# Kernel optimization log

Hardware: AMD Instinct MI355X
Metric: run time of the kernel (lower is better)

## Reference

```python
import jax, jax.numpy as jnp
import numpy as np

B, L, H, D = 4, 2048, 12, 64
CHUNK = 128  # chunk size for the causal linear-attention scan
EPS = 1e-6


def setup_inputs() -> dict:
    key = jax.random.key(0)
    kq, kk, kv = jax.random.split(key, 3)
    return {
        "q": jax.random.normal(kq, (B, L, H, D), jnp.float32),
        "k": jax.random.normal(kk, (B, L, H, D), jnp.float32),
        "v": jax.random.normal(kv, (B, L, H, D), jnp.float32),
    }


def _phi(x):
    # elu feature map: elu(x) + 1 (strictly positive)
    return jax.nn.elu(x) + 1.0


def _causal_linear(q, k, v):
    """Chunked causal linear attention numerator.
    out[l] = q[l] @ sum_{s<=l} k[s] (x) v[s].  q,k,v: [N,L,H,D]."""
    n, l, h, d = q.shape
    g = l // CHUNK
    qc = q.reshape(n, g, CHUNK, h, d)
    kc = k.reshape(n, g, CHUNK, h, d)
    vc = v.reshape(n, g, CHUNK, h, d)
    # per-chunk kv outer-product sums -> [N, G, H, D, M]
    kv = jnp.einsum('ngchd,ngchm->nghdm', kc, vc)
    # exclusive prefix sum over chunks (state entering each chunk)
    s_incl = jnp.cumsum(kv, axis=1)
    s_excl = jnp.concatenate([jnp.zeros_like(s_incl[:, :1]), s_incl[:, :-1]], axis=1)
    inter = jnp.einsum('ngchd,nghdm->ngchm', qc, s_excl)
    # intra-chunk causal part
    scores = jnp.einsum('ngchd,ngshd->ngchs', qc, kc)  # [N,G,C,H,C]
    mask = jnp.tril(jnp.ones((CHUNK, CHUNK), scores.dtype))  # s <= c
    scores = scores * mask.reshape(1, 1, CHUNK, 1, CHUNK)
    intra = jnp.einsum('ngchs,ngshm->ngchm', scores, vc)
    return (inter + intra).reshape(n, l, h, -1)


def reference(q, k, v):
    qf = _phi(q)
    kf = _phi(k)
    # normalizer z[n,l,h] = q[l] . cumsum_s<=l k[s]
    z = jnp.einsum('nlhd,nlhd->nlh', qf, jnp.cumsum(kf, axis=1)) + EPS
    num = _causal_linear(qf, kf, v)
    return num / z[..., None]
```

## Files before the change

### kernel.cpp

```cpp
#include <hip/hip_runtime.h>

#define NB 4
#define LL 2048
#define NH 12
#define DD 64
#define CB 128
#define NG (LL/CB)
#define NBH (NB*NH)
#define ST_BYTES (DD*DD*2)
#define KS_BASE_BYTES ((size_t)NBH*NG*ST_BYTES)

typedef short bf16x8 __attribute__((ext_vector_type(8)));
typedef float f32x4  __attribute__((ext_vector_type(4)));

#define SWZ8(row, x)  ((x) ^ (((row) & 7) << 4))
#define SWZ16(row, x) ((x) ^ (((row) & 15) << 4))

__device__ __forceinline__ float phi(float x) {
    return x > 0.0f ? x + 1.0f : __expf(x);
}
__device__ __forceinline__ unsigned f2bf1(float x) {
    union { float f; unsigned u; } v; v.f = x;
    return (v.u + 0x7FFFu + ((v.u >> 16) & 1u)) >> 16;
}
__device__ __forceinline__ unsigned packbf(float a, float b) {
    return f2bf1(a) | (f2bf1(b) << 16);
}
__device__ __forceinline__ float bf2f(unsigned short u) {
    union { unsigned u; float f; } v; v.u = ((unsigned)u) << 16; return v.f;
}
__device__ __forceinline__ void addbf8(float* run, uint4 a) {
    const unsigned u[4] = {a.x, a.y, a.z, a.w};
    #pragma unroll
    for (int i = 0; i < 4; ++i) {
        run[2*i+0] += bf2f((unsigned short)(u[i] & 0xffffu));
        run[2*i+1] += bf2f((unsigned short)(u[i] >> 16));
    }
}
__device__ __forceinline__ uint4 pack8(const float* run) {
    uint4 s;
    s.x = packbf(run[0], run[1]); s.y = packbf(run[2], run[3]);
    s.z = packbf(run[4], run[5]); s.w = packbf(run[6], run[7]);
    return s;
}

__global__ __launch_bounds__(256) void la_chunk_sums(
    const float* __restrict__ kin, const float* __restrict__ vin,
    char* __restrict__ wsb)
{
    __shared__ __align__(16) char sm[32768];
    const int bid = blockIdx.x;
    const int g = bid & (NG-1);
    const int h = (bid >> 4) % NH;
    const int n = bid / (NG*NH);
    const int t = threadIdx.x;
    const int l0 = g * CB;
    const int w = t >> 6, l = t & 63, gq = l >> 4, c16 = l & 15;

    #pragma unroll
    for (int p = 0; p < 8; ++p) {
        const int i = p*256 + t;
        const int r = i >> 4, c4 = i & 15;
        const size_t gidx = ((size_t)((n*LL + l0 + r)*NH + h))*DD + c4*4;
        float4 kk = *(const float4*)(kin + gidx);
        float4 vl = *(const float4*)(vin + gidx);
        const float kf[4] = {phi(kk.x), phi(kk.y), phi(kk.z), phi(kk.w)};
        const float vf[4] = {vl.x, vl.y, vl.z, vl.w};
        #pragma unroll
        for (int j = 0; j < 4; ++j) {
            const int d = c4*4 + j;
            *(unsigned short*)(sm +         d*256 + SWZ16(d, 2*r)) = (unsigned short)f2bf1(kf[j]);
            *(unsigned short*)(sm + 16384 + d*256 + SWZ16(d, 2*r)) = (unsigned short)f2bf1(vf[j]);
        }
    }
    __syncthreads();

    const int m = 16*w + c16;
    bf16x8 va[4];
    #pragma unroll
    for (int ks = 0; ks < 4; ++ks)
        va[ks] = *(const bf16x8*)(sm + 16384 + m*256 + SWZ16(m, 64*ks + 16*gq));
    const short one = (short)0x3F80;
    const bf16x8 ones = {one, one, one, one, one, one, one, one};

    f32x4 acc[4], ksa[4];
    #pragma unroll
    for (int td = 0; td < 4; ++td) {
        acc[td] = (f32x4){0.f,0.f,0.f,0.f};
        ksa[td] = (f32x4){0.f,0.f,0.f,0.f};
    }
    #pragma unroll
    for (int td = 0; td < 4; ++td) {
        const int d = 16*td + c16;
        #pragma unroll
        for (int ks = 0; ks < 4; ++ks) {
            const bf16x8 kb = *(const bf16x8*)(sm + d*256 + SWZ16(d, 64*ks + 16*gq));
            acc[td] = __builtin_amdgcn_mfma_f32_16x16x32_bf16(va[ks], kb, acc[td], 0, 0, 0);
            ksa[td] = __builtin_amdgcn_mfma_f32_16x16x32_bf16(ones,  kb, ksa[td], 0, 0, 0);
        }
    }

    char* stg = wsb + (size_t)bid * ST_BYTES;
    #pragma unroll
    for (int td = 0; td < 4; ++td)
        #pragma unroll
        for (int e = 0; e < 4; ++e) {
            const int mr = 16*w + 4*gq + e;
            const int d  = 16*td + c16;
            *(unsigned short*)(stg + mr*128 + d*2) = (unsigned short)f2bf1(acc[td][e]);
        }
    if (w == 0 && gq == 0) {
        float* ksw = (float*)(wsb + KS_BASE_BYTES) + (size_t)bid * DD;
        #pragma unroll
        for (int td = 0; td < 4; ++td)
            ksw[16*td + c16] = ksa[td][0];
    }
}

__global__ __launch_bounds__(256) void la_scan(char* __restrict__ wsb)
{
    const int nh = blockIdx.x / 3;
    const int sl = blockIdx.x % 3;
    const int t  = threadIdx.x;
    if (sl < 2) {
        const int t4 = sl*256 + t;
        char* base = wsb + (size_t)nh * NG * ST_BYTES + (size_t)t4 * 16;
        float run[8];
        #pragma unroll
        for (int i = 0; i < 8; ++i) run[i] = 0.f;
        #pragma unroll
        for (int g2 = 0; g2 < NG; g2 += 2) {
            uint4 a0 = *(uint4*)(base + (size_t)(g2+0)*ST_BYTES);
            uint4 a1 = *(uint4*)(base + (size_t)(g2+1)*ST_BYTES);
            *(uint4*)(base + (size_t)(g2+0)*ST_BYTES) = pack8(run);
            addbf8(run, a0);
            *(uint4*)(base + (size_t)(g2+1)*ST_BYTES) = pack8(run);
            addbf8(run, a1);
        }
    } else if (t < DD) {
        float* base = (float*)(wsb + KS_BASE_BYTES) + (size_t)nh * NG * DD + t;
        float run = 0.f;
        #pragma unroll
        for (int g4 = 0; g4 < NG; g4 += 4) {
            float a0 = base[(g4+0)*DD], a1 = base[(g4+1)*DD];
            float a2 = base[(g4+2)*DD], a3 = base[(g4+3)*DD];
            base[(g4+0)*DD] = run; run += a0;
            base[(g4+1)*DD] = run; run += a1;
            base[(g4+2)*DD] = run; run += a2;
            base[(g4+3)*DD] = run; run += a3;
        }
    }
}

#define SM_Q   0
#define SM_K   16384
#define SM_S   0
#define SM_VT  32768
#define SM_STX 49152
#define SM_KSX 57344
#define SM_ZL  57600
#define SM_BYTES 58112

__global__ __launch_bounds__(512) void la_output(
    const float* __restrict__ qin, const float* __restrict__ kin,
    const float* __restrict__ vin, const char* __restrict__ wsb,
    float* __restrict__ out)
{
    __shared__ __align__(16) char sm[SM_BYTES];
    const int bid = blockIdx.x;
    const int g = bid & (NG-1);
    const int h = (bid >> 4) % NH;
    const int n = bid / (NG*NH);
    const int t = threadIdx.x;
    const int l0 = g * CB;
    const int w = t >> 6, l = t & 63, gq = l >> 4, c16 = l & 15;
    const int c = 16*w + c16;

    #pragma unroll
    for (int p = 0; p < 4; ++p) {
        const int i = p*512 + t;
        const int r = i >> 4, c4 = i & 15;
        const size_t gidx = ((size_t)((n*LL + l0 + r)*NH + h))*DD + c4*4;
        float4 qq = *(const float4*)(qin + gidx);
        float4 kk = *(const float4*)(kin + gidx);
        float4 vl = *(const float4*)(vin + gidx);
        uint2 qp; qp.x = packbf(phi(qq.x), phi(qq.y)); qp.y = packbf(phi(qq.z), phi(qq.w));
        uint2 kp; kp.x = packbf(phi(kk.x), phi(kk.y)); kp.y = packbf(phi(kk.z), phi(kk.w));
        *(uint2*)(sm + SM_Q + r*128 + SWZ8(r, c4*8)) = qp;
        *(uint2*)(sm + SM_K + r*128 + SWZ8(r, c4*8)) = kp;
        const float vf[4] = {vl.x, vl.y, vl.z, vl.w};
        #pragma unroll
        for (int j = 0; j < 4; ++j) {
            const int m = c4*4 + j;
            *(unsigned short*)(sm + SM_VT + m*256 + SWZ16(m, 2*r)) = (unsigned short)f2bf1(vf[j]);
        }
    }
    {
        const char* stg = wsb + (size_t)bid * ST_BYTES;
        const int mr = t >> 3, cc = t & 7;
        *(uint4*)(sm + SM_STX + mr*128 + SWZ8(mr, cc*16)) = *(const uint4*)(stg + mr*128 + cc*16);
    }
    if (t < DD)
        ((float*)(sm + SM_KSX))[t] =
            ((const float*)(wsb + KS_BASE_BYTES))[(size_t)bid * DD + t];
    __syncthreads();

    const bf16x8 qf0 = *(const bf16x8*)(sm + SM_Q + c*128 + SWZ8(c, 16*gq));
    const bf16x8 qf1 = *(const bf16x8*)(sm + SM_Q + c*128 + SWZ8(c, 64 + 16*gq));

    f32x4 sreg[8];
    #pragma unroll
    for (int tr = 0; tr < 8; ++tr) {
        const int r = 16*tr + c16;
        const bf16x8 ka0 = *(const bf16x8*)(sm + SM_K + r*128 + SWZ8(r, 16*gq));
        const bf16x8 ka1 = *(const bf16x8*)(sm + SM_K + r*128 + SWZ8(r, 64 + 16*gq));
        f32x4 a; a[0]=0.f; a[1]=0.f; a[2]=0.f; a[3]=0.f;
        a = __builtin_amdgcn_mfma_f32_16x16x32_bf16(ka0, qf0, a, 0, 0, 0);
        a = __builtin_amdgcn_mfma_f32_16x16x32_bf16(ka1, qf1, a, 0, 0, 0);
        sreg[tr] = a;
    }
    float z = 0.f;
    #pragma unroll
    for (int tr = 0; tr < 8; ++tr)
        #pragma unroll
        for (int e = 0; e < 4; ++e) {
            const int rr = 16*tr + 4*gq + e;
            if (rr <= c) z += sreg[tr][e]; else sreg[tr][e] = 0.f;
        }
    {
        const float* ksxf = (const float*)(sm + SM_KSX);
        #pragma unroll
        for (int i = 0; i < 8; ++i) {
            z += bf2f((unsigned short)qf0[i]) * ksxf[8*gq + i];
            z += bf2f((unsigned short)qf1[i]) * ksxf[32 + 8*gq + i];
        }
    }
    z += __shfl_xor(z, 16);
    z += __shfl_xor(z, 32);
    __syncthreads();

    #pragma unroll
    for (int tr = 0; tr < 8; ++tr) {
        uint2 sp; sp.x = packbf(sreg[tr][0], sreg[tr][1]); sp.y = packbf(sreg[tr][2], sreg[tr][3]);
        *(uint2*)(sm + SM_S + c*256 + SWZ16(c, 32*tr + 8*gq)) = sp;
    }
    if (gq == 0) ((float*)(sm + SM_ZL))[c] = z;
    __syncthreads();

    bf16x8 sf[4];
    #pragma unroll
    for (int ks = 0; ks < 4; ++ks)
        sf[ks] = *(const bf16x8*)(sm + SM_S + c*256 + SWZ16(c, 64*ks + 16*gq));
    f32x4 acc[4];
    #pragma unroll
    for (int tm = 0; tm < 4; ++tm) { acc[tm][0]=0.f; acc[tm][1]=0.f; acc[tm][2]=0.f; acc[tm][3]=0.f; }
    #pragma unroll
    for (int tm = 0; tm < 4; ++tm) {
        const int m = 16*tm + c16;
        #pragma unroll
        for (int ks = 0; ks < 4; ++ks) {
            const bf16x8 vf = *(const bf16x8*)(sm + SM_VT + m*256 + SWZ16(m, 64*ks + 16*gq));
            acc[tm] = __builtin_amdgcn_mfma_f32_16x16x32_bf16(sf[ks], vf, acc[tm], 0, 0, 0);
        }
        const bf16x8 st0 = *(const bf16x8*)(sm + SM_STX + m*128 + SWZ8(m, 16*gq));
        const bf16x8 st1 = *(const bf16x8*)(sm + SM_STX + m*128 + SWZ8(m, 64 + 16*gq));
        acc[tm] = __builtin_amdgcn_mfma_f32_16x16x32_bf16(qf0, st0, acc[tm], 0, 0, 0);
        acc[tm] = __builtin_amdgcn_mfma_f32_16x16x32_bf16(qf1, st1, acc[tm], 0, 0, 0);
    }

    float zinv[4];
    #pragma unroll
    for (int e = 0; e < 4; ++e) {
        const float zr = ((const float*)(sm + SM_ZL))[16*w + 4*gq + e];
        zinv[e] = 1.0f / (zr + 1e-6f);
    }
    #pragma unroll
    for (int tm = 0; tm < 4; ++tm)
        #pragma unroll
        for (int e = 0; e < 4; ++e) {
            const int cr = 16*w + 4*gq + e;
            const int m  = 16*tm + c16;
            out[((size_t)((n*LL + l0 + cr)*NH + h))*DD + m] = acc[tm][e] * zinv[e];
        }
}

extern "C" void kernel_launch(void* const* d_in, const int* in_sizes, int n_in,
                              void* d_out, int out_size, void* d_ws, size_t ws_size,
                              hipStream_t stream) {
    const float* q = (const float*)d_in[0];
    const float* k = (const float*)d_in[1];
    const float* v = (const float*)d_in[2];
    float* out = (float*)d_out;
    char* wsb  = (char*)d_ws;

    const int nblk = NB * NH * NG;
    la_chunk_sums<<<nblk, 256, 0, stream>>>(k, v, wsb);
    la_scan<<<NBH*3, 256, 0, stream>>>(wsb);
    la_output<<<nblk, 512, 0, stream>>>(q, k, v, wsb, out);
}
```

Baseline: 40.67 us.

## Stage bf16 phi(k) and transposed v in workspace for reuse by output kernel

The chunk-sums kernel now writes its bf16 swizzled phi(k) tile and transposed bf16 v tile to workspace. The output kernel copies these straight into shared memory instead of re-reading fp32 k and v and recomputing phi and the transposes. The scan also writes the exclusive prefix state pre-swizzled into a separate buffer, so the output kernel can do a flat copy. This halves the global bytes read for k and v in the output pass, in exchange for extra workspace writes in the first kernel and a larger workspace footprint.

```diff
diff --git a/kernel.cpp b/kernel.cpp
--- a/kernel.cpp
+++ b/kernel.cpp
@@ -8,7 +8,12 @@
 #define NG (LL/CB)
 #define NBH (NB*NH)
 #define ST_BYTES (DD*DD*2)
-#define KS_BASE_BYTES ((size_t)NBH*NG*ST_BYTES)
+
+#define ST2_OFF   ((size_t)NBH*NG*ST_BYTES)
+#define KS_OFF    (ST2_OFF + (size_t)NBH*NG*ST_BYTES)
+#define KPRE_OFF  (KS_OFF + (size_t)NBH*NG*DD*4)
+#define PRE_BYTES ((size_t)16384)
+#define VTPRE_OFF (KPRE_OFF + (size_t)NBH*NG*PRE_BYTES)
 
 typedef short bf16x8 __attribute__((ext_vector_type(8)));
 typedef float f32x4  __attribute__((ext_vector_type(4)));
@@ -57,6 +62,9 @@
     const int l0 = g * CB;
     const int w = t >> 6, l = t & 63, gq = l >> 4, c16 = l & 15;
 
+    char* kpre  = wsb + KPRE_OFF  + (size_t)bid * PRE_BYTES;
+    char* vtpre = wsb + VTPRE_OFF + (size_t)bid * PRE_BYTES;
+
     #pragma unroll
     for (int p = 0; p < 8; ++p) {
         const int i = p*256 + t;
@@ -66,6 +74,8 @@
         float4 vl = *(const float4*)(vin + gidx);
         const float kf[4] = {phi(kk.x), phi(kk.y), phi(kk.z), phi(kk.w)};
         const float vf[4] = {vl.x, vl.y, vl.z, vl.w};
+        uint2 kp; kp.x = packbf(kf[0], kf[1]); kp.y = packbf(kf[2], kf[3]);
+        *(uint2*)(kpre + r*128 + SWZ8(r, c4*8)) = kp;
         #pragma unroll
         for (int j = 0; j < 4; ++j) {
             const int d = c4*4 + j;
@@ -100,6 +110,12 @@
         }
     }
 
+    #pragma unroll
+    for (int p = 0; p < 4; ++p) {
+        const int i = p*256 + t;
+        *(uint4*)(vtpre + i*16) = *(const uint4*)(sm + 16384 + i*16);
+    }
+
     char* stg = wsb + (size_t)bid * ST_BYTES;
     #pragma unroll
     for (int td = 0; td < 4; ++td)
@@ -110,7 +126,7 @@
             *(unsigned short*)(stg + mr*128 + d*2) = (unsigned short)f2bf1(acc[td][e]);
         }
     if (w == 0 && gq == 0) {
-        float* ksw = (float*)(wsb + KS_BASE_BYTES) + (size_t)bid * DD;
+        float* ksw = (float*)(wsb + KS_OFF) + (size_t)bid * DD;
         #pragma unroll
         for (int td = 0; td < 4; ++td)
             ksw[16*td + c16] = ksa[td][0];
@@ -124,21 +140,24 @@
     const int t  = threadIdx.x;
     if (sl < 2) {
         const int t4 = sl*256 + t;
-        char* base = wsb + (size_t)nh * NG * ST_BYTES + (size_t)t4 * 16;
+        const int mr = t4 >> 3, cc = t4 & 7;
+        const char* rbase = wsb + (size_t)nh * NG * ST_BYTES + (size_t)t4 * 16;
+        char*       wbase = wsb + ST2_OFF + (size_t)nh * NG * ST_BYTES
+                            + mr*128 + SWZ8(mr, cc*16);
         float run[8];
         #pragma unroll
         for (int i = 0; i < 8; ++i) run[i] = 0.f;
         #pragma unroll
         for (int g2 = 0; g2 < NG; g2 += 2) {
-            uint4 a0 = *(uint4*)(base + (size_t)(g2+0)*ST_BYTES);
-            uint4 a1 = *(uint4*)(base + (size_t)(g2+1)*ST_BYTES);
-            *(uint4*)(base + (size_t)(g2+0)*ST_BYTES) = pack8(run);
+            uint4 a0 = *(const uint4*)(rbase + (size_t)(g2+0)*ST_BYTES);
+            uint4 a1 = *(const uint4*)(rbase + (size_t)(g2+1)*ST_BYTES);
+            *(uint4*)(wbase + (size_t)(g2+0)*ST_BYTES) = pack8(run);
             addbf8(run, a0);
-            *(uint4*)(base + (size_t)(g2+1)*ST_BYTES) = pack8(run);
+            *(uint4*)(wbase + (size_t)(g2+1)*ST_BYTES) = pack8(run);
             addbf8(run, a1);
         }
     } else if (t < DD) {
-        float* base = (float*)(wsb + KS_BASE_BYTES) + (size_t)nh * NG * DD + t;
+        float* base = (float*)(wsb + KS_OFF) + (size_t)nh * NG * DD + t;
         float run = 0.f;
         #pragma unroll
         for (int g4 = 0; g4 < NG; g4 += 4) {
@@ -162,8 +181,7 @@
 #define SM_BYTES 58112
 
 __global__ __launch_bounds__(512) void la_output(
-    const float* __restrict__ qin, const float* __restrict__ kin,
-    const float* __restrict__ vin, const char* __restrict__ wsb,
+    const float* __restrict__ qin, const char* __restrict__ wsb,
     float* __restrict__ out)
 {
     __shared__ __align__(16) char sm[SM_BYTES];
@@ -182,27 +200,24 @@
         const int r = i >> 4, c4 = i & 15;
         const size_t gidx = ((size_t)((n*LL + l0 + r)*NH + h))*DD + c4*4;
         float4 qq = *(const float4*)(qin + gidx);
-        float4 kk = *(const float4*)(kin + gidx);
-        float4 vl = *(const float4*)(vin + gidx);
         uint2 qp; qp.x = packbf(phi(qq.x), phi(qq.y)); qp.y = packbf(phi(qq.z), phi(qq.w));
-        uint2 kp; kp.x = packbf(phi(kk.x), phi(kk.y)); kp.y = packbf(phi(kk.z), phi(kk.w));
         *(uint2*)(sm + SM_Q + r*128 + SWZ8(r, c4*8)) = qp;
-        *(uint2*)(sm + SM_K + r*128 + SWZ8(r, c4*8)) = kp;
-        const float vf[4] = {vl.x, vl.y, vl.z, vl.w};
-        #pragma unroll
-        for (int j = 0; j < 4; ++j) {
-            const int m = c4*4 + j;
-            *(unsigned short*)(sm + SM_VT + m*256 + SWZ16(m, 2*r)) = (unsigned short)f2bf1(vf[j]);
-        }
     }
     {
-        const char* stg = wsb + (size_t)bid * ST_BYTES;
-        const int mr = t >> 3, cc = t & 7;
-        *(uint4*)(sm + SM_STX + mr*128 + SWZ8(mr, cc*16)) = *(const uint4*)(stg + mr*128 + cc*16);
+        const char* kpre  = wsb + KPRE_OFF  + (size_t)bid * PRE_BYTES;
+        const char* vtpre = wsb + VTPRE_OFF + (size_t)bid * PRE_BYTES;
+        const char* st2   = wsb + ST2_OFF   + (size_t)bid * ST_BYTES;
+        #pragma unroll
+        for (int p = 0; p < 2; ++p) {
+            const int i = (p*512 + t) * 16;
+            *(uint4*)(sm + SM_K  + i) = *(const uint4*)(kpre  + i);
+            *(uint4*)(sm + SM_VT + i) = *(const uint4*)(vtpre + i);
+        }
+        *(uint4*)(sm + SM_STX + t*16) = *(const uint4*)(st2 + t*16);
     }
     if (t < DD)
         ((float*)(sm + SM_KSX))[t] =
-            ((const float*)(wsb + KS_BASE_BYTES))[(size_t)bid * DD + t];
+            ((const float*)(wsb + KS_OFF))[(size_t)bid * DD + t];
     __syncthreads();
 
     const bf16x8 qf0 = *(const bf16x8*)(sm + SM_Q + c*128 + SWZ8(c, 16*gq));
@@ -296,5 +311,5 @@
     const int nblk = NB * NH * NG;
     la_chunk_sums<<<nblk, 256, 0, stream>>>(k, v, wsb);
     la_scan<<<NBH*3, 256, 0, stream>>>(wsb);
-    la_output<<<nblk, 512, 0, stream>>>(q, k, v, wsb, out);
-}
+    la_output<<<nblk, 512, 0, stream>>>(q, wsb, out);
+}
```

New measurement: 45.11 us. 10.9% more time.

## Fuse chunk-state prefix scan into output kernel, dropping separate scan launch

Applied to the files above, without the earlier changes.

Removes the la_scan kernel. Each output block now sums the per-chunk KV states and k-sums of all earlier chunks itself to form its exclusive prefix state. This saves one kernel launch and a global read/write pass, at the cost of redundant work: block g reads g chunk states, so total state reads grow quadratically with chunk count (up to 15 extra 8KB reads per block).

```diff
diff --git a/kernel.cpp b/kernel.cpp
--- a/kernel.cpp
+++ b/kernel.cpp
@@ -117,41 +117,6 @@
     }
 }
 
-__global__ __launch_bounds__(256) void la_scan(char* __restrict__ wsb)
-{
-    const int nh = blockIdx.x / 3;
-    const int sl = blockIdx.x % 3;
-    const int t  = threadIdx.x;
-    if (sl < 2) {
-        const int t4 = sl*256 + t;
-        char* base = wsb + (size_t)nh * NG * ST_BYTES + (size_t)t4 * 16;
-        float run[8];
-        #pragma unroll
-        for (int i = 0; i < 8; ++i) run[i] = 0.f;
-        #pragma unroll
-        for (int g2 = 0; g2 < NG; g2 += 2) {
-            uint4 a0 = *(uint4*)(base + (size_t)(g2+0)*ST_BYTES);
-            uint4 a1 = *(uint4*)(base + (size_t)(g2+1)*ST_BYTES);
-            *(uint4*)(base + (size_t)(g2+0)*ST_BYTES) = pack8(run);
-            addbf8(run, a0);
-            *(uint4*)(base + (size_t)(g2+1)*ST_BYTES) = pack8(run);
-            addbf8(run, a1);
-        }
-    } else if (t < DD) {
-        float* base = (float*)(wsb + KS_BASE_BYTES) + (size_t)nh * NG * DD + t;
-        float run = 0.f;
-        #pragma unroll
-        for (int g4 = 0; g4 < NG; g4 += 4) {
-            float a0 = base[(g4+0)*DD], a1 = base[(g4+1)*DD];
-            float a2 = base[(g4+2)*DD], a3 = base[(g4+3)*DD];
-            base[(g4+0)*DD] = run; run += a0;
-            base[(g4+1)*DD] = run; run += a1;
-            base[(g4+2)*DD] = run; run += a2;
-            base[(g4+3)*DD] = run; run += a3;
-        }
-    }
-}
-
 #define SM_Q   0
 #define SM_K   16384
 #define SM_S   0
@@ -171,6 +136,7 @@
     const int g = bid & (NG-1);
     const int h = (bid >> 4) % NH;
     const int n = bid / (NG*NH);
+    const int nh = n*NH + h;
     const int t = threadIdx.x;
     const int l0 = g * CB;
     const int w = t >> 6, l = t & 63, gq = l >> 4, c16 = l & 15;
@@ -196,13 +162,21 @@
         }
     }
     {
-        const char* stg = wsb + (size_t)bid * ST_BYTES;
         const int mr = t >> 3, cc = t & 7;
-        *(uint4*)(sm + SM_STX + mr*128 + SWZ8(mr, cc*16)) = *(const uint4*)(stg + mr*128 + cc*16);
-    }
-    if (t < DD)
-        ((float*)(sm + SM_KSX))[t] =
-            ((const float*)(wsb + KS_BASE_BYTES))[(size_t)bid * DD + t];
+        float run[8];
+        #pragma unroll
+        for (int i = 0; i < 8; ++i) run[i] = 0.f;
+        const char* stb = wsb + (size_t)nh * NG * ST_BYTES + mr*128 + cc*16;
+        for (int gg = 0; gg < g; ++gg)
+            addbf8(run, *(const uint4*)(stb + (size_t)gg * ST_BYTES));
+        *(uint4*)(sm + SM_STX + mr*128 + SWZ8(mr, cc*16)) = pack8(run);
+    }
+    if (t < DD) {
+        const float* ksb = (const float*)(wsb + KS_BASE_BYTES) + (size_t)nh * NG * DD + t;
+        float run = 0.f;
+        for (int gg = 0; gg < g; ++gg) run += ksb[(size_t)gg * DD];
+        ((float*)(sm + SM_KSX))[t] = run;
+    }
     __syncthreads();
 
     const bf16x8 qf0 = *(const bf16x8*)(sm + SM_Q + c*128 + SWZ8(c, 16*gq));
@@ -295,6 +269,5 @@
 
     const int nblk = NB * NH * NG;
     la_chunk_sums<<<nblk, 256, 0, stream>>>(k, v, wsb);
-    la_scan<<<NBH*3, 256, 0, stream>>>(wsb);
     la_output<<<nblk, 512, 0, stream>>>(q, k, v, wsb, out);
 }
```

Result: slower. 48.38 us (+18.9%).
